# Kernel optimization log

Hardware: AMD Instinct MI355X
Metric: run time of the kernel (lower is better)

The kernel has to match this reference:

```python
import jax, jax.numpy as jnp
import numpy as np
from jax import lax

B, C, H, W = 8, 256, 128, 128
RED = 4  # SE reduction


def setup_inputs() -> dict:
    key = jax.random.key(0)
    ks = jax.random.split(key, 7)
    s = 0.05
    return {
        "x": jax.random.normal(ks[0], (B, C, H, W), dtype=jnp.float32),
        "w_deform": jax.random.normal(ks[1], (C, C, 3, 3), dtype=jnp.float32) * s,
        "b_deform": jax.random.normal(ks[2], (C,), dtype=jnp.float32) * s,
        "w_se1": jax.random.normal(ks[3], (C // RED, C), dtype=jnp.float32) * s,
        "b_se1": jax.random.normal(ks[4], (C // RED,), dtype=jnp.float32) * s,
        "w_se2": jax.random.normal(ks[5], (C, C // RED), dtype=jnp.float32) * s,
        "b_se2": jax.random.normal(ks[6], (C,), dtype=jnp.float32) * s,
    }


def reference(x, w_deform, b_deform, w_se1, b_se1, w_se2, b_se2):
    # DeformConv2d with the all-zero offset tensor used in forward(): bilinear
    # sampling at integer taps == standard 3x3 conv, padding=1, zero-padded borders.
    y = lax.conv_general_dilated(
        x, w_deform,
        window_strides=(1, 1),
        padding=((1, 1), (1, 1)),
        dimension_numbers=("NCHW", "OIHW", "NCHW"),
    ) + b_deform[None, :, None, None]  # [B, C, H, W]

    # SE: global average pool -> 1x1 conv -> ReLU -> 1x1 conv -> sigmoid
    p = y.mean(axis=(2, 3))                                   # [B, C]
    h = jax.nn.relu(p @ w_se1.T + b_se1)                      # [B, C//RED]
    scale = jax.nn.sigmoid(h @ w_se2.T + b_se2)               # [B, C]
    return y * scale[:, :, None, None]
```

## Files before the change

### kernel.cpp

```cpp
#include <hip/hip_runtime.h>
#include <hip/hip_bf16.h>

#define BB 8
#define CC 256
#define HH 128
#define WW 128

typedef __attribute__((ext_vector_type(8))) short bf16x8;
typedef __attribute__((ext_vector_type(4))) float f32x4;

static __device__ __forceinline__ unsigned short f2bf(float f) {
  unsigned int u = __builtin_bit_cast(unsigned int, f);
  u += 0x7fffu + ((u >> 16) & 1u);
  return (unsigned short)(u >> 16);
}

static __device__ __forceinline__ void async16(const void* g, void* l) {
#if __has_builtin(__builtin_amdgcn_global_load_lds)
  __builtin_amdgcn_global_load_lds(
      (__attribute__((address_space(1))) void*)(unsigned long long)(g),
      (__attribute__((address_space(3))) void*)(unsigned int)(unsigned long long)(l),
      16, 0, 0);
#else
  *(bf16x8*)l = *(const bf16x8*)g;
#endif
}

__global__ __launch_bounds__(256) void k_convert_w(const float* __restrict__ w,
                                                   unsigned short* __restrict__ Wt,
                                                   float* __restrict__ sums) {
  __shared__ unsigned short lw[8 * 2304];
  const int t = threadIdx.x;
  const int co0 = blockIdx.x << 3;
  for (int z = blockIdx.x * 256 + t; z < 18432; z += 8192) sums[z] = 0.f;
  const float* src = w + co0 * 2304;
  for (int k = t; k < 18432; k += 256) lw[k] = f2bf(src[k]);
  __syncthreads();
  for (int g = t; g < 18432; g += 256) {
    const int tap = g >> 11, rem = g & 2047;
    const int o = rem >> 6, rem2 = rem & 63;
    const int cl = rem2 >> 3, e = rem2 & 7;
    Wt[(((tap << 5) + o) << 11) + ((co0 + cl) << 3) + e] =
        lw[cl * 2304 + ((o << 3) + e) * 9 + tap];
  }
}

__global__ __launch_bounds__(256) void k_transpose_x(const float* __restrict__ x,
                                                     unsigned short* __restrict__ Xc,
                                                     float* __restrict__ sums) {
  __shared__ float tile[64][65];
  const int t = threadIdx.x;
  const int bz = blockIdx.z;
  const int b = bz >> 7, h = bz & 127;
  const int c0 = blockIdx.y << 6, w0 = blockIdx.x << 6;
  const float* xp = x + (((b * CC) * HH) + h) * WW;
#pragma unroll
  for (int i = 0; i < 4; ++i) {
    int idx = t + (i << 8);
    int cr = idx >> 4, wq = idx & 15;
    float4 v = *(const float4*)(xp + (c0 + cr) * (HH * WW) + w0 + (wq << 2));
    tile[cr][(wq << 2) + 0] = v.x;
    tile[cr][(wq << 2) + 1] = v.y;
    tile[cr][(wq << 2) + 2] = v.z;
    tile[cr][(wq << 2) + 3] = v.w;
  }
  __syncthreads();
  const int ob = c0 >> 3;
#pragma unroll
  for (int i = 0; i < 2; ++i) {
    int g = t + (i << 8);
    int o = g >> 6, wr = g & 63;
    bf16x8 v;
#pragma unroll
    for (int e = 0; e < 8; ++e) v[e] = (short)f2bf(tile[(o << 3) + e][wr]);
    *(bf16x8*)(Xc + ((((b << 7) + h) * 32) + ob + o) * 1024 + (w0 + wr) * 8) = v;
  }
  {
    const int c = t >> 2, seg = t & 3;
    float s = 0.f;
#pragma unroll
    for (int k = 0; k < 16; ++k) s += tile[c][(seg << 4) + k];
    s += __shfl_xor(s, 1);
    s += __shfl_xor(s, 2);
    const int ci = b * CC + c0 + c;
    if (seg == 0) {
      atomicAdd(&sums[ci], s);
      if (h == 0)   atomicAdd(&sums[2048 + ci], s);
      if (h == 127) atomicAdd(&sums[4096 + ci], s);
      if (w0 == 0) {
        atomicAdd(&sums[6144 + ci], tile[c][0]);
        if (h == 0)   atomicAdd(&sums[10240 + ci], tile[c][0]);
        if (h == 127) atomicAdd(&sums[14336 + ci], tile[c][0]);
      }
    }
    if (seg == 3 && w0 == 64) {
      atomicAdd(&sums[8192 + ci], tile[c][63]);
      if (h == 0)   atomicAdd(&sums[12288 + ci], tile[c][63]);
      if (h == 127) atomicAdd(&sums[16384 + ci], tile[c][63]);
    }
  }
}

__global__ __launch_bounds__(256) void k_pool2(const float* __restrict__ w,
                                               const float* __restrict__ bd,
                                               const float* __restrict__ sums,
                                               float* __restrict__ p_buf) {
  __shared__ float ts[2304];
  const int b = blockIdx.y, t = threadIdx.x;
  const int lane = t & 63, wid = t >> 6;
  {
    const int ci = (b << 8) + t;
    const float S  = sums[ci];
    const float R0 = sums[2048 + ci], R1 = sums[4096 + ci];
    const float C0 = sums[6144 + ci], C1 = sums[8192 + ci];
    const float x00 = sums[10240 + ci], x0W = sums[12288 + ci];
    const float xH0 = sums[14336 + ci], xHW = sums[16384 + ci];
    const float er[3] = {R1, 0.f, R0};
    const float ec[3] = {C1, 0.f, C0};
    const float cor[9] = {xHW, 0.f, xH0, 0.f, 0.f, 0.f, x0W, 0.f, x00};
#pragma unroll
    for (int kh = 0; kh < 3; ++kh)
#pragma unroll
      for (int kw = 0; kw < 3; ++kw)
        ts[t * 9 + kh * 3 + kw] = S - er[kh] - ec[kw] + cor[kh * 3 + kw];
  }
  __syncthreads();
  float4 tv[9];
#pragma unroll
  for (int q = 0; q < 9; ++q) tv[q] = *(const float4*)&ts[(q * 64 + lane) * 4];
  const int co = (blockIdx.x << 3) + (wid << 1);
#pragma unroll
  for (int c2 = 0; c2 < 2; ++c2) {
    const float4* wr = (const float4*)(w + (co + c2) * 2304) + lane;
    float s = 0.f;
#pragma unroll
    for (int q = 0; q < 9; ++q) {
      float4 wv = wr[q * 64];
      s += wv.x * tv[q].x + wv.y * tv[q].y + wv.z * tv[q].z + wv.w * tv[q].w;
    }
    s += __shfl_xor(s, 1);  s += __shfl_xor(s, 2);  s += __shfl_xor(s, 4);
    s += __shfl_xor(s, 8);  s += __shfl_xor(s, 16); s += __shfl_xor(s, 32);
    if (lane == 0) p_buf[(b << 8) + co + c2] = bd[co + c2] + s * (1.0f / 16384.0f);
  }
}

__global__ __launch_bounds__(256) void k_se2(const float* __restrict__ p_buf,
                                             const float* __restrict__ w1,
                                             const float* __restrict__ b1,
                                             const float* __restrict__ w2,
                                             const float* __restrict__ b2,
                                             float* __restrict__ scale) {
  __shared__ float p[CC];
  __shared__ float h1[64];
  const int b = blockIdx.x, t = threadIdx.x;
  const int lane = t & 63, wid = t >> 6;
  p[t] = p_buf[(b << 8) + t];
  __syncthreads();
  {
    const float4 pv = *(const float4*)&p[lane << 2];
#pragma unroll
    for (int i = 0; i < 16; ++i) {
      const int r = (wid << 4) + i;
      float4 wv = ((const float4*)(w1 + (r << 8)))[lane];
      float s = wv.x * pv.x + wv.y * pv.y + wv.z * pv.z + wv.w * pv.w;
      s += __shfl_xor(s, 1);  s += __shfl_xor(s, 2);  s += __shfl_xor(s, 4);
      s += __shfl_xor(s, 8);  s += __shfl_xor(s, 16); s += __shfl_xor(s, 32);
      if (lane == 0) {
        float v = b1[r] + s;
        h1[r] = v > 0.f ? v : 0.f;
      }
    }
  }
  __syncthreads();
  {
    float s = b2[t];
    const float* wr = w2 + (t << 6);
#pragma unroll
    for (int k = 0; k < 64; ++k) s += wr[k] * h1[k];
    scale[(b << 8) + t] = 1.0f / (1.0f + expf(-s));
  }
}

__global__ __launch_bounds__(256, 2) void k_conv(
    const unsigned short* __restrict__ Xc, const unsigned short* __restrict__ Wt,
    const float* __restrict__ bias, const float* __restrict__ scale,
    float* __restrict__ out) {
  extern __shared__ __align__(16) unsigned short Xs[];
  const int t = threadIdx.x;
  const int lin = (blockIdx.y << 1) | blockIdx.x;
  const int Wk = ((lin & 7) << 7) | (lin >> 3);
  const int m0 = (Wk & 1) << 7;
  const int bhp = Wk >> 1;
  const int b = bhp >> 6;
  const int h0 = (bhp & 63) << 1;
  const int lane = t & 63, wid = t >> 6;
  const int wave_m = (wid & 1) << 6, wave_n = (wid >> 1) << 6;
  const int n0 = lane & 15, quad = lane >> 4;
  const int part = wid & 1, rsel = wid >> 1;

  bf16x8 z8 = {0, 0, 0, 0, 0, 0, 0, 0};
  if (t < 64) {
    int bi = t >> 5, rem = t & 31;
    int dh = rem >> 3, rem2 = rem & 7, q = rem2 >> 1, side = rem2 & 1;
    *(bf16x8*)&Xs[bi * 16640 + dh * 4160 + q * 1040 + (side ? 1032 : 0)] = z8;
  }
  if (h0 == 0 || h0 == 126) {
    const int dhz = (h0 == 0) ? 0 : 3;
    for (int g = t; g < 1040; g += 256) {
      int bi = g >= 520, gg = g - bi * 520;
      *(bf16x8*)&Xs[bi * 16640 + dhz * 4160 + gg * 8] = z8;
    }
  }

  auto stage = [&](int cb8, int bi) {
    const int ob = cb8 << 2;
#pragma unroll
    for (int r = 0; r < 8; ++r) {
      const int rr = (r << 1) | rsel;
      const int dh = rr >> 2, q = rr & 3;
      const int hh = h0 - 1 + dh;
      if (hh >= 0 && hh < HH) {
        const unsigned short* gp =
            Xc + ((((b << 7) + hh) * 32 + ob + q) << 10) + (part << 9) + (lane << 3);
        unsigned short* lp =
            &Xs[bi * 16640 + dh * 4160 + q * 1040 + 8 + (part << 9) + (lane << 3)];
        async16(gp, lp);
      }
    }
  };

  f32x4 acc[2][4][4];
  f32x4 zero4 = {0.f, 0.f, 0.f, 0.f};
#pragma unroll
  for (int r = 0; r < 2; ++r)
#pragma unroll
    for (int i = 0; i < 4; ++i)
#pragma unroll
      for (int j = 0; j < 4; ++j) acc[r][i][j] = zero4;

  stage(0, 0);
  __syncthreads();

  for (int cb8 = 0; cb8 < 8; ++cb8) {
    const int cur = cb8 & 1;
    if (cb8 < 7) stage(cb8 + 1, cur ^ 1);
    const unsigned short* wb =
        Wt + ((((cb8 << 2) + quad) << 8) + m0 + wave_m + n0) * 8;
    const unsigned short* xb = &Xs[cur * 16640 + quad * 1040 + (wave_n + n0) * 8];

    bf16x8 af[2][4], bg[2][4];
#pragma unroll
    for (int i = 0; i < 4; ++i) af[0][i] = *(const bf16x8*)(wb + i * 128);
#pragma unroll
    for (int j = 0; j < 4; ++j) bg[0][j] = *(const bf16x8*)(xb + (j << 4) * 8);

#pragma unroll
    for (int t9 = 0; t9 < 9; ++t9) {
#pragma unroll
      for (int r2 = 0; r2 < 2; ++r2) {
        const int s = t9 * 2 + r2;
        if (s < 17) {
          const int sn = s + 1;
          const int rn = sn & 1, tn = sn >> 1;
          const int khn = tn / 3, kwn = tn % 3;
#pragma unroll
          for (int j = 0; j < 4; ++j)
            bg[sn & 1][j] =
                *(const bf16x8*)(xb + (rn + khn) * 4160 + ((j << 4) + kwn) * 8);
        }
        if (r2 == 0 && t9 < 8) {
#pragma unroll
          for (int i = 0; i < 4; ++i)
            af[(t9 + 1) & 1][i] =
                *(const bf16x8*)(wb + (t9 + 1) * 65536 + i * 128);
        }
#pragma unroll
        for (int i = 0; i < 4; ++i)
#pragma unroll
          for (int j = 0; j < 4; ++j)
            acc[r2][i][j] = __builtin_amdgcn_mfma_f32_16x16x32_bf16(
                af[t9 & 1][i], bg[s & 1][j], acc[r2][i][j], 0, 0, 0);
      }
    }
    __syncthreads();
  }

#pragma unroll
  for (int i = 0; i < 4; ++i) {
    const int mrow = m0 + wave_m + (i << 4) + (quad << 2);
    float bs[4], ss[4];
#pragma unroll
    for (int r4 = 0; r4 < 4; ++r4) {
      bs[r4] = bias[mrow + r4];
      ss[r4] = scale[(b << 8) + mrow + r4];
    }
#pragma unroll
    for (int r = 0; r < 2; ++r)
#pragma unroll
      for (int j = 0; j < 4; ++j) {
        const int wcol = wave_n + (j << 4) + n0;
        float* op = out + ((((b << 8) + mrow) * HH) + h0 + r) * WW + wcol;
#pragma unroll
        for (int r4 = 0; r4 < 4; ++r4)
          op[r4 * (HH * WW)] = (acc[r][i][j][r4] + bs[r4]) * ss[r4];
      }
  }
}

extern "C" void kernel_launch(void* const* d_in, const int* in_sizes, int n_in,
                              void* d_out, int out_size, void* d_ws, size_t ws_size,
                              hipStream_t stream) {
  const float* x  = (const float*)d_in[0];
  const float* wd = (const float*)d_in[1];
  const float* bd = (const float*)d_in[2];
  const float* w1 = (const float*)d_in[3];
  const float* b1 = (const float*)d_in[4];
  const float* w2 = (const float*)d_in[5];
  const float* b2 = (const float*)d_in[6];
  float* out = (float*)d_out;

  char* ws = (char*)d_ws;
  unsigned short* Xc = (unsigned short*)ws;
  unsigned short* Wt = (unsigned short*)(ws + 67108864);
  float* sums  = (float*)(ws + 68288512);
  float* p_buf = (float*)(ws + 68362240);
  float* scale = (float*)(ws + 68370432);

  (void)hipFuncSetAttribute((const void*)k_conv,
                            hipFuncAttributeMaxDynamicSharedMemorySize, 66560);

  k_convert_w<<<dim3(32), dim3(256), 0, stream>>>(wd, Wt, sums);
  k_transpose_x<<<dim3(2, 4, 1024), dim3(256), 0, stream>>>(x, Xc, sums);
  k_pool2<<<dim3(32, 8), dim3(256), 0, stream>>>(wd, bd, sums, p_buf);
  k_se2<<<dim3(8), dim3(256), 0, stream>>>(p_buf, w1, b1, w2, b2, scale);
  k_conv<<<dim3(2, 512), dim3(256), 66560, stream>>>(Xc, Wt, bd, scale, out);
}
```

Before: 389.4 us.

## Reorder conv tap loop by kernel column to share input fragments across rows

The inner loop now goes over kernel columns and four input row offsets instead of nine taps times two output rows. Each loaded input fragment feeds both output-row accumulators, so 12 LDS loads of B fragments replace 18. Weight fragments use a three-deep rotating buffer in the new tap order, prefetched further ahead. The cost is extra registers for the third weight buffer and more intricate indexing.

```diff
diff --git a/kernel.cpp b/kernel.cpp
--- a/kernel.cpp
+++ b/kernel.cpp
@@ -248,38 +248,51 @@
         Wt + ((((cb8 << 2) + quad) << 8) + m0 + wave_m + n0) * 8;
     const unsigned short* xb = &Xs[cur * 16640 + quad * 1040 + (wave_n + n0) * 8];
 
-    bf16x8 af[2][4], bg[2][4];
-#pragma unroll
-    for (int i = 0; i < 4; ++i) af[0][i] = *(const bf16x8*)(wb + i * 128);
+    bf16x8 af[3][4], bg[2][4];
+#pragma unroll
+    for (int i = 0; i < 4; ++i) af[0][i] = *(const bf16x8*)(wb + 0 * 65536 + i * 128);
+#pragma unroll
+    for (int i = 0; i < 4; ++i) af[1][i] = *(const bf16x8*)(wb + 3 * 65536 + i * 128);
 #pragma unroll
     for (int j = 0; j < 4; ++j) bg[0][j] = *(const bf16x8*)(xb + (j << 4) * 8);
 
 #pragma unroll
-    for (int t9 = 0; t9 < 9; ++t9) {
-#pragma unroll
-      for (int r2 = 0; r2 < 2; ++r2) {
-        const int s = t9 * 2 + r2;
-        if (s < 17) {
-          const int sn = s + 1;
-          const int rn = sn & 1, tn = sn >> 1;
-          const int khn = tn / 3, kwn = tn % 3;
+    for (int kw = 0; kw < 3; ++kw) {
+#pragma unroll
+      for (int dh = 0; dh < 4; ++dh) {
+        const int s = (kw << 2) + dh;
+        if (s < 11) {
+          const int sn = s + 1, kwn = sn >> 2, dhn = sn & 3;
 #pragma unroll
           for (int j = 0; j < 4; ++j)
             bg[sn & 1][j] =
-                *(const bf16x8*)(xb + (rn + khn) * 4160 + ((j << 4) + kwn) * 8);
+                *(const bf16x8*)(xb + dhn * 4160 + (((j << 4) + kwn)) * 8);
         }
-        if (r2 == 0 && t9 < 8) {
+        if (dh >= 1) {
+          const int p1 = kw * 3 + dh - 1;
 #pragma unroll
           for (int i = 0; i < 4; ++i)
-            af[(t9 + 1) & 1][i] =
-                *(const bf16x8*)(wb + (t9 + 1) * 65536 + i * 128);
+#pragma unroll
+            for (int j = 0; j < 4; ++j)
+              acc[1][i][j] = __builtin_amdgcn_mfma_f32_16x16x32_bf16(
+                  af[p1 % 3][i], bg[s & 1][j], acc[1][i][j], 0, 0, 0);
         }
-#pragma unroll
-        for (int i = 0; i < 4; ++i)
-#pragma unroll
-          for (int j = 0; j < 4; ++j)
-            acc[r2][i][j] = __builtin_amdgcn_mfma_f32_16x16x32_bf16(
-                af[t9 & 1][i], bg[s & 1][j], acc[r2][i][j], 0, 0, 0);
+        if (dh <= 2) {
+          const int p0 = kw * 3 + dh;
+#pragma unroll
+          for (int i = 0; i < 4; ++i)
+#pragma unroll
+            for (int j = 0; j < 4; ++j)
+              acc[0][i][j] = __builtin_amdgcn_mfma_f32_16x16x32_bf16(
+                  af[p0 % 3][i], bg[s & 1][j], acc[0][i][j], 0, 0, 0);
+        }
+        if (s >= 1 && s <= 7) {
+          const int pn = s + 1;
+          const int tapn = (pn % 3) * 3 + pn / 3;
+#pragma unroll
+          for (int i = 0; i < 4; ++i)
+            af[pn % 3][i] = *(const bf16x8*)(wb + tapn * 65536 + i * 128);
+        }
       }
     }
     __syncthreads();
```

Result: no change. 382.9 us (-1.7%).
